# Kernel optimization log

Hardware: AMD Instinct MI355X
Metric: run time of the kernel (lower is better)

Reference implementation:

```python
import jax, jax.numpy as jnp
import numpy as np

IN_DIM = 28 * 28   # 784, hard-coded in the torch module
HIDDEN = 1024
OUT_DIM = 10
BATCH = 256
P_KEEP = 0.5       # torch.bernoulli(p * ones) -> keep probability p


def setup_inputs() -> dict:
    key = jax.random.key(0)
    ks = jax.random.split(key, 8)
    x = jax.random.normal(ks[0], (BATCH, IN_DIM), dtype=jnp.float32)
    # Bernoulli(p) mask over (out, in, batch), as in drop_connect
    mask = (jax.random.uniform(ks[1], (HIDDEN, IN_DIM, BATCH)) < P_KEEP).astype(jnp.float32)
    # xavier_uniform with relu gain = sqrt(2)
    def xavier(k, fan_out, fan_in):
        gain = np.sqrt(2.0)
        bound = gain * np.sqrt(6.0 / (fan_in + fan_out))
        return jax.random.uniform(k, (fan_out, fan_in), minval=-bound, maxval=bound, dtype=jnp.float32)
    W1 = xavier(ks[2], HIDDEN, IN_DIM)
    b1 = jnp.zeros((HIDDEN,), jnp.float32)
    W2 = xavier(ks[3], HIDDEN, HIDDEN)
    b2 = jnp.zeros((HIDDEN,), jnp.float32)
    W3 = xavier(ks[4], OUT_DIM, HIDDEN)
    b3 = jnp.zeros((OUT_DIM,), jnp.float32)
    return {"x": x, "mask": mask, "W1": W1, "b1": b1, "W2": W2, "b2": b2, "W3": W3, "b3": b3}


def reference(x, mask, W1, b1, W2, b2, W3, b3):
    # DropConnect layer 1: per-sample masked weight.
    # torch loop: result[b] = (W1 * mask[:, :, b]) @ x[b] + b1
    h1 = jnp.einsum('hi,hib,bi->bh', W1, mask, x) + b1   # [B, H]
    h1 = jax.nn.relu(h1)
    h2 = jax.nn.relu(h1 @ W2.T + b2)                      # [B, H]
    out = h2 @ W3.T + b3                                  # [B, 10]
    return out
```

## Files before the change

kernel.cpp:

```cpp
#include <hip/hip_runtime.h>
#include <hip/hip_bf16.h>

#define IN_DIM 784
#define HIDDEN 1024
#define OUT_DIM 10
#define BATCH 256

__global__ __launch_bounds__(256) void k_transpose_x(
    const float* __restrict__ x, float* __restrict__ xT)
{
    const int i = blockIdx.x;
    const int b = threadIdx.x;
    xT[i * BATCH + b] = x[b * IN_DIM + i];
}

__global__ __launch_bounds__(256) void k_layer1(
    const float* __restrict__ W1, const float* __restrict__ mask,
    const float* __restrict__ xT, const float* __restrict__ b1,
    float* __restrict__ h1T)
{
    const int h  = blockIdx.x;
    const int t  = threadIdx.x;
    const int bg = t & 63;
    const int is = t >> 6;

    const float4* __restrict__ mask4 =
        (const float4*)(mask + (size_t)h * (IN_DIM * BATCH));
    const float4* __restrict__ xT4 = (const float4*)xT;
    const float* __restrict__ w1row = W1 + h * IN_DIM;

    float4 acc = make_float4(0.f, 0.f, 0.f, 0.f);
    #pragma unroll 4
    for (int i = is; i < IN_DIM; i += 4) {
        const float  w = w1row[i];
        const float4 m = mask4[i * 64 + bg];
        const float4 xv = xT4[i * 64 + bg];
        acc.x = fmaf(w, m.x * xv.x, acc.x);
        acc.y = fmaf(w, m.y * xv.y, acc.y);
        acc.z = fmaf(w, m.z * xv.z, acc.z);
        acc.w = fmaf(w, m.w * xv.w, acc.w);
    }

    __shared__ float4 red[4][64];
    red[is][bg] = acc;
    __syncthreads();
    if (is == 0) {
        const float4 s0 = red[0][bg], s1 = red[1][bg];
        const float4 s2 = red[2][bg], s3 = red[3][bg];
        const float bias = b1[h];
        float4 r;
        r.x = fmaxf(s0.x + s1.x + s2.x + s3.x + bias, 0.f);
        r.y = fmaxf(s0.y + s1.y + s2.y + s3.y + bias, 0.f);
        r.z = fmaxf(s0.z + s1.z + s2.z + s3.z + bias, 0.f);
        r.w = fmaxf(s0.w + s1.w + s2.w + s3.w + bias, 0.f);
        ((float4*)h1T)[h * 64 + bg] = r;
    }
}

__global__ __launch_bounds__(256) void k_layer2(
    const float* __restrict__ h1T, const float* __restrict__ W2,
    const float* __restrict__ b2, float* __restrict__ h2)
{
    const int t  = threadIdx.x;
    const int jj = t & 31;
    const int bg = t >> 5;
    const int b0 = blockIdx.x * 32;
    const int j0 = blockIdx.y * 32;

    __shared__ __align__(16) float Ash[32][32];
    __shared__ float Bsh[32][33];

    float acc0 = 0.f, acc1 = 0.f, acc2 = 0.f, acc3 = 0.f;

    for (int h0 = 0; h0 < HIDDEN; h0 += 32) {
        #pragma unroll
        for (int r = 0; r < 4; r++) {
            const int idx = t + r * 256;
            const int hh = idx >> 5, bb = idx & 31;
            Ash[hh][bb] = h1T[(h0 + hh) * BATCH + b0 + bb];
        }
        #pragma unroll
        for (int r = 0; r < 4; r++) {
            const int idx = t + r * 256;
            const int jl = idx >> 5, hl = idx & 31;
            Bsh[hl][jl] = W2[(j0 + jl) * HIDDEN + h0 + hl];
        }
        __syncthreads();
        #pragma unroll 8
        for (int hh = 0; hh < 32; hh++) {
            const float w = Bsh[hh][jj];
            const float4 a = *(const float4*)&Ash[hh][bg * 4];
            acc0 = fmaf(a.x, w, acc0);
            acc1 = fmaf(a.y, w, acc1);
            acc2 = fmaf(a.z, w, acc2);
            acc3 = fmaf(a.w, w, acc3);
        }
        __syncthreads();
    }

    const float bias = b2[j0 + jj];
    const int base = (b0 + bg * 4) * HIDDEN + j0 + jj;
    h2[base + 0 * HIDDEN] = fmaxf(acc0 + bias, 0.f);
    h2[base + 1 * HIDDEN] = fmaxf(acc1 + bias, 0.f);
    h2[base + 2 * HIDDEN] = fmaxf(acc2 + bias, 0.f);
    h2[base + 3 * HIDDEN] = fmaxf(acc3 + bias, 0.f);
}

__global__ __launch_bounds__(256) void k_layer3(
    const float* __restrict__ h2, const float* __restrict__ W3,
    const float* __restrict__ b3, float* __restrict__ out)
{
    const int b = blockIdx.x;
    const int t = threadIdx.x;
    const int lane = t & 63, wid = t >> 6;

    __shared__ float hbuf[HIDDEN];
    #pragma unroll
    for (int r = 0; r < 4; r++)
        hbuf[t + r * 256] = h2[b * HIDDEN + t + r * 256];
    __syncthreads();

    float acc[OUT_DIM];
    #pragma unroll
    for (int o = 0; o < OUT_DIM; o++) acc[o] = 0.f;

    for (int h = t; h < HIDDEN; h += 256) {
        const float v = hbuf[h];
        #pragma unroll
        for (int o = 0; o < OUT_DIM; o++)
            acc[o] = fmaf(v, W3[o * HIDDEN + h], acc[o]);
    }

    __shared__ float red[4][OUT_DIM];
    #pragma unroll
    for (int o = 0; o < OUT_DIM; o++) {
        float v = acc[o];
        for (int off = 32; off > 0; off >>= 1)
            v += __shfl_down(v, off);
        if (lane == 0) red[wid][o] = v;
    }
    __syncthreads();
    if (t < OUT_DIM) {
        out[b * OUT_DIM + t] =
            red[0][t] + red[1][t] + red[2][t] + red[3][t] + b3[t];
    }
}

extern "C" void kernel_launch(void* const* d_in, const int* in_sizes, int n_in,
                              void* d_out, int out_size, void* d_ws, size_t ws_size,
                              hipStream_t stream) {
    const float* x    = (const float*)d_in[0];
    const float* mask = (const float*)d_in[1];
    const float* W1   = (const float*)d_in[2];
    const float* b1   = (const float*)d_in[3];
    const float* W2   = (const float*)d_in[4];
    const float* b2   = (const float*)d_in[5];
    const float* W3   = (const float*)d_in[6];
    const float* b3   = (const float*)d_in[7];
    float* out = (float*)d_out;

    float* ws  = (float*)d_ws;
    float* xT  = ws;
    float* h1T = xT + IN_DIM * BATCH;
    float* h2  = h1T + HIDDEN * BATCH;

    k_transpose_x<<<IN_DIM, 256, 0, stream>>>(x, xT);
    k_layer1<<<HIDDEN, 256, 0, stream>>>(W1, mask, xT, b1, h1T);
    k_layer2<<<dim3(BATCH / 32, HIDDEN / 32), 256, 0, stream>>>(h1T, W2, b2, h2);
    k_layer3<<<BATCH, 256, 0, stream>>>(h2, W3, b3, out);
}
```

Before: 1.084 ms.

## Split layer-1 over input chunks with shared-memory x/W1 tiles and separate reduce

Layer 1 is restructured so each 1024-thread block handles 32 hidden units over a 49-wide input chunk. The chunk's xT and W1 slices are staged in shared memory, and the mask stream is read with nontemporal loads. Per-chunk partial sums go to a workspace buffer and a new reduce kernel adds bias and applies ReLU. The aim is to cut redundant xT/W1 global reads and improve streaming of the 800MB mask, at the cost of an extra kernel launch and the partial-sum traffic.

```diff
diff --git a/kernel.cpp b/kernel.cpp
--- a/kernel.cpp
+++ b/kernel.cpp
@@ -6,6 +6,12 @@
 #define OUT_DIM 10
 #define BATCH 256
 
+#define C_I 49
+#define N_CH 16
+#define H_T 32
+
+typedef float __attribute__((ext_vector_type(4))) f32x4;
+
 __global__ __launch_bounds__(256) void k_transpose_x(
     const float* __restrict__ x, float* __restrict__ xT)
 {
@@ -14,47 +20,88 @@
     xT[i * BATCH + b] = x[b * IN_DIM + i];
 }
 
-__global__ __launch_bounds__(256) void k_layer1(
+__global__ __launch_bounds__(1024, 8) void k_layer1_split(
     const float* __restrict__ W1, const float* __restrict__ mask,
-    const float* __restrict__ xT, const float* __restrict__ b1,
+    const float* __restrict__ xT, float* __restrict__ partial)
+{
+    const int ht   = blockIdx.x;
+    const int c    = blockIdx.y;
+    const int h0   = ht * H_T;
+    const int i0   = c * C_I;
+    const int t    = threadIdx.x;
+    const int bg   = t & 63;
+    const int slot = t >> 6;
+
+    __shared__ f32x4 xs[C_I][64];
+    __shared__ float wsh[H_T][C_I];
+
+    {
+        const f32x4* src = (const f32x4*)(xT + i0 * BATCH);
+        f32x4* dst = &xs[0][0];
+        for (int idx = t; idx < C_I * 64; idx += 1024)
+            dst[idx] = src[idx];
+    }
+    {
+        float* dst = &wsh[0][0];
+        for (int idx = t; idx < H_T * C_I; idx += 1024) {
+            const int hh = idx / C_I, ii = idx - hh * C_I;
+            dst[idx] = W1[(h0 + hh) * IN_DIM + i0 + ii];
+        }
+    }
+    __syncthreads();
+
+    f32x4 acc[2];
+    #pragma unroll
+    for (int k = 0; k < 2; k++) {
+        const int hh = slot * 2 + k;
+        const int h  = h0 + hh;
+        const f32x4* mrow =
+            (const f32x4*)(mask + ((size_t)h * IN_DIM + i0) * BATCH) + bg;
+        f32x4 a = {0.f, 0.f, 0.f, 0.f};
+        #pragma unroll 2
+        for (int i = 0; i < C_I; i++) {
+            const f32x4 m  = __builtin_nontemporal_load(mrow + i * 64);
+            const f32x4 xv = xs[i][bg];
+            const float w  = wsh[hh][i];
+            a.x = fmaf(w, m.x * xv.x, a.x);
+            a.y = fmaf(w, m.y * xv.y, a.y);
+            a.z = fmaf(w, m.z * xv.z, a.z);
+            a.w = fmaf(w, m.w * xv.w, a.w);
+        }
+        acc[k] = a;
+    }
+
+    #pragma unroll
+    for (int k = 0; k < 2; k++) {
+        const int h = h0 + slot * 2 + k;
+        __builtin_nontemporal_store(
+            acc[k], (f32x4*)partial + ((size_t)c * HIDDEN + h) * 64 + bg);
+    }
+}
+
+__global__ __launch_bounds__(256) void k_reduce_h1(
+    const float* __restrict__ partial, const float* __restrict__ b1,
     float* __restrict__ h1T)
 {
-    const int h  = blockIdx.x;
     const int t  = threadIdx.x;
     const int bg = t & 63;
-    const int is = t >> 6;
-
-    const float4* __restrict__ mask4 =
-        (const float4*)(mask + (size_t)h * (IN_DIM * BATCH));
-    const float4* __restrict__ xT4 = (const float4*)xT;
-    const float* __restrict__ w1row = W1 + h * IN_DIM;
-
-    float4 acc = make_float4(0.f, 0.f, 0.f, 0.f);
-    #pragma unroll 4
-    for (int i = is; i < IN_DIM; i += 4) {
-        const float  w = w1row[i];
-        const float4 m = mask4[i * 64 + bg];
-        const float4 xv = xT4[i * 64 + bg];
-        acc.x = fmaf(w, m.x * xv.x, acc.x);
-        acc.y = fmaf(w, m.y * xv.y, acc.y);
-        acc.z = fmaf(w, m.z * xv.z, acc.z);
-        acc.w = fmaf(w, m.w * xv.w, acc.w);
-    }
-
-    __shared__ float4 red[4][64];
-    red[is][bg] = acc;
-    __syncthreads();
-    if (is == 0) {
-        const float4 s0 = red[0][bg], s1 = red[1][bg];
-        const float4 s2 = red[2][bg], s3 = red[3][bg];
-        const float bias = b1[h];
-        float4 r;
-        r.x = fmaxf(s0.x + s1.x + s2.x + s3.x + bias, 0.f);
-        r.y = fmaxf(s0.y + s1.y + s2.y + s3.y + bias, 0.f);
-        r.z = fmaxf(s0.z + s1.z + s2.z + s3.z + bias, 0.f);
-        r.w = fmaxf(s0.w + s1.w + s2.w + s3.w + bias, 0.f);
-        ((float4*)h1T)[h * 64 + bg] = r;
-    }
+    const int h  = blockIdx.x * 4 + (t >> 6);
+
+    const f32x4* p4 = (const f32x4*)partial;
+    f32x4 s = {0.f, 0.f, 0.f, 0.f};
+    #pragma unroll
+    for (int cc = 0; cc < N_CH; cc++) {
+        const f32x4 v = __builtin_nontemporal_load(
+            p4 + ((size_t)cc * HIDDEN + h) * 64 + bg);
+        s.x += v.x; s.y += v.y; s.z += v.z; s.w += v.w;
+    }
+    const float b = b1[h];
+    f32x4 r;
+    r.x = fmaxf(s.x + b, 0.f);
+    r.y = fmaxf(s.y + b, 0.f);
+    r.z = fmaxf(s.z + b, 0.f);
+    r.w = fmaxf(s.w + b, 0.f);
+    ((f32x4*)h1T)[h * 64 + bg] = r;
 }
 
 __global__ __launch_bounds__(256) void k_layer2(
@@ -159,13 +206,15 @@
     const float* b3   = (const float*)d_in[7];
     float* out = (float*)d_out;
 
-    float* ws  = (float*)d_ws;
-    float* xT  = ws;
-    float* h1T = xT + IN_DIM * BATCH;
-    float* h2  = h1T + HIDDEN * BATCH;
+    float* ws      = (float*)d_ws;
+    float* xT      = ws;
+    float* h1T     = xT + IN_DIM * BATCH;
+    float* h2      = h1T + HIDDEN * BATCH;
+    float* partial = h2 + BATCH * HIDDEN;
 
     k_transpose_x<<<IN_DIM, 256, 0, stream>>>(x, xT);
-    k_layer1<<<HIDDEN, 256, 0, stream>>>(W1, mask, xT, b1, h1T);
+    k_layer1_split<<<dim3(HIDDEN / H_T, N_CH), 1024, 0, stream>>>(W1, mask, xT, partial);
+    k_reduce_h1<<<HIDDEN / 4, 256, 0, stream>>>(partial, b1, h1T);
     k_layer2<<<dim3(BATCH / 32, HIDDEN / 32), 256, 0, stream>>>(h1T, W2, b2, h2);
     k_layer3<<<BATCH, 256, 0, stream>>>(h2, W3, b3, out);
 }
```

Result: faster. 1.051 ms (-3.0%).
